# Performance work log

Measured on AMD Instinct MI355X. Metric: run time of the kernel, lower is better.

## Reference

```python
import jax, jax.numpy as jnp
import numpy as np

B, T, D, H, O = 64, 512, 512, 512, 1

def setup_inputs() -> dict:
    key = jax.random.key(0)
    ks = jax.random.split(key, 12)
    s_in = 1.0 / np.sqrt(H)
    inp = {
        'x': jax.random.normal(ks[0], (B, T, D), dtype=jnp.float32),
        'W_ih0': jax.random.uniform(ks[1], (H, D), jnp.float32, -s_in, s_in),
        'W_hh0': jax.random.uniform(ks[2], (H, H), jnp.float32, -s_in, s_in),
        'b_ih0': jax.random.uniform(ks[3], (H,), jnp.float32, -s_in, s_in),
        'b_hh0': jax.random.uniform(ks[4], (H,), jnp.float32, -s_in, s_in),
        'W_ih1': jax.random.uniform(ks[5], (H, H), jnp.float32, -s_in, s_in),
        'W_hh1': jax.random.uniform(ks[6], (H, H), jnp.float32, -s_in, s_in),
        'b_ih1': jax.random.uniform(ks[7], (H,), jnp.float32, -s_in, s_in),
        'b_hh1': jax.random.uniform(ks[8], (H,), jnp.float32, -s_in, s_in),
        'W_fc': jax.random.uniform(ks[9], (O, H), jnp.float32, -s_in, s_in),
        'b_fc': jax.random.uniform(ks[10], (O,), jnp.float32, -s_in, s_in),
    }
    return inp

def _rnn_layer(inp, W_ih, W_hh, b_ih, b_hh):
    # inp: [B, T, Din] -> [B, T, H].  h_t = tanh(x_t W_ih^T + b_ih + h_{t-1} W_hh^T + b_hh)
    xproj = jnp.einsum('btd,hd->bth', inp, W_ih) + b_ih + b_hh  # precompute input projection
    h0 = jnp.zeros((inp.shape[0], W_hh.shape[0]), inp.dtype)
    def step(h, xp):  # xp: [B, H]
        h = jnp.tanh(xp + h @ W_hh.T)
        return h, h
    _, outs = jax.lax.scan(step, h0, jnp.swapaxes(xproj, 0, 1))  # [T, B, H]
    return jnp.swapaxes(outs, 0, 1)

def reference(x, W_ih0, W_hh0, b_ih0, b_hh0, W_ih1, W_hh1, b_ih1, b_hh1, W_fc, b_fc):
    h = _rnn_layer(x, W_ih0, W_hh0, b_ih0, b_hh0)
    h = _rnn_layer(h, W_ih1, W_hh1, b_ih1, b_hh1)
    last = h[:, -1, :]                      # [B, H]
    return last @ W_fc.T + b_fc             # [B, O]
```

## Files before the change

kernel.cpp:

```cpp
#include <hip/hip_runtime.h>
#include <cstdint>
#include <cstddef>

typedef _Float16 f16;
typedef _Float16 half2_t __attribute__((ext_vector_type(2)));
typedef _Float16 half4_t __attribute__((ext_vector_type(4)));
typedef _Float16 half8_t __attribute__((ext_vector_type(8)));
typedef float floatx4 __attribute__((ext_vector_type(4)));

__device__ __forceinline__ float fdot2u(uint32_t w, uint32_t h, float acc) {
#if __has_builtin(__builtin_amdgcn_fdot2)
    return __builtin_amdgcn_fdot2(__builtin_bit_cast(half2_t, w),
                                  __builtin_bit_cast(half2_t, h), acc, false);
#else
    half2_t a = __builtin_bit_cast(half2_t, w);
    half2_t b = __builtin_bit_cast(half2_t, h);
    return acc + (float)a[0] * (float)b[0] + (float)a[1] * (float)b[1];
#endif
}

__device__ __forceinline__ void spin_ge(int* f, int v) {
    while (__hip_atomic_load(f, __ATOMIC_RELAXED, __HIP_MEMORY_SCOPE_AGENT) < v)
        __builtin_amdgcn_s_sleep(16);
}

__global__ void cvt_kernel(const float* __restrict__ in, f16* __restrict__ out, int n4) {
    int i = blockIdx.x * blockDim.x + threadIdx.x;
    int stride = gridDim.x * blockDim.x;
    const float4* in4 = (const float4*)in;
    half4_t* out4 = (half4_t*)out;
    for (; i < n4; i += stride) {
        float4 v = in4[i];
        half4_t h = {(f16)v.x, (f16)v.y, (f16)v.z, (f16)v.w};
        out4[i] = h;
    }
}

__global__ void bsum_kernel(const float* __restrict__ a, const float* __restrict__ b,
                            float* __restrict__ o) {
    int i = threadIdx.x;
    o[i] = a[i] + b[i];
}

__global__ void pack_whh(const float* __restrict__ W, uint32_t* __restrict__ wp) {
    int id = blockIdx.x * 256 + threadIdx.x;
    int j = id >> 8;
    int kp = id & 255;
    int k = kp * 2;
    int w = j >> 6, jsub = (j >> 3) & 7, r = j & 7;
    int kg = k >> 6, c = (k >> 3) & 7, q = (k >> 1) & 3;
    int tid = w * 64 + jsub * 8 + kg;
    int idx = c * 32 + r * 4 + q;
    uint32_t lo = (uint32_t)__builtin_bit_cast(uint16_t, (f16)W[(size_t)j * 512 + k]);
    uint32_t hi = (uint32_t)__builtin_bit_cast(uint16_t, (f16)W[(size_t)j * 512 + k + 1]);
    size_t off;
    if (idx < 224) off = (size_t)idx * 512 + tid;
    else           off = (size_t)224 * 512 + ((size_t)(r * 512 + tid)) * 4 + q;
    wp[off] = (hi << 16) | lo;
}

__global__ __launch_bounds__(256) void gemm_xp(const f16* __restrict__ A,
                                               const f16* __restrict__ Bw,
                                               const float* __restrict__ bias,
                                               f16* __restrict__ C) {
    const int bn = blockIdx.x & 3;
    const int bm = blockIdx.x >> 2;
    const int tid = threadIdx.x;
    const int w = tid >> 6, l = tid & 63;
    const int wr = w >> 1, wc = w & 1;
    __shared__ f16 As[128 * 32];
    __shared__ f16 Bs[128 * 32];
    floatx4 acc[4][4] = {};
    const int lr = l & 15, lk = (l >> 4) * 8;
    for (int kk = 0; kk < 512; kk += 32) {
        __syncthreads();
        uint4 av[2], bv[2];
#pragma unroll
        for (int s = 0; s < 2; ++s) {
            int chunk = tid + s * 256;
            int row = chunk >> 2;
            int colh = (chunk & 3) * 8;
            av[s] = *(const uint4*)&A[((size_t)(bm * 128 + row)) * 512 + kk + colh];
            bv[s] = *(const uint4*)&Bw[((size_t)(bn * 128 + row)) * 512 + kk + colh];
        }
#pragma unroll
        for (int s = 0; s < 2; ++s) {
            int chunk = tid + s * 256;
            *(uint4*)&As[chunk * 8] = av[s];
            *(uint4*)&Bs[chunk * 8] = bv[s];
        }
        __syncthreads();
        half8_t af[4], bf[4];
#pragma unroll
        for (int m = 0; m < 4; ++m)
            af[m] = *(const half8_t*)&As[(wr * 64 + m * 16 + lr) * 32 + lk];
#pragma unroll
        for (int n = 0; n < 4; ++n)
            bf[n] = *(const half8_t*)&Bs[(wc * 64 + n * 16 + lr) * 32 + lk];
#pragma unroll
        for (int m = 0; m < 4; ++m)
#pragma unroll
            for (int n = 0; n < 4; ++n)
                acc[m][n] = __builtin_amdgcn_mfma_f32_16x16x32_f16(af[m], bf[n], acc[m][n], 0, 0, 0);
    }
    float bz[4];
#pragma unroll
    for (int n = 0; n < 4; ++n) bz[n] = bias[bn * 128 + wc * 64 + n * 16 + lr];
    const int lq = l >> 4;
#pragma unroll
    for (int m = 0; m < 4; ++m)
#pragma unroll
        for (int n = 0; n < 4; ++n)
#pragma unroll
            for (int e = 0; e < 4; ++e) {
                int row = bm * 128 + wr * 64 + m * 16 + lq * 4 + e;
                int col = bn * 128 + wc * 64 + n * 16 + lr;
                C[(size_t)row * 512 + col] = (f16)(acc[m][n][e] + bz[n]);
            }
}

#define FOR_Q(M, c, r) M(c, r, 0) M(c, r, 1) M(c, r, 2) M(c, r, 3)
#define FOR_R8(M, c) FOR_Q(M, c, 0) FOR_Q(M, c, 1) FOR_Q(M, c, 2) FOR_Q(M, c, 3) \
                     FOR_Q(M, c, 4) FOR_Q(M, c, 5) FOR_Q(M, c, 6) FOR_Q(M, c, 7)
#define FOR_ALL(M) FOR_R8(M, 0) FOR_R8(M, 1) FOR_R8(M, 2) FOR_R8(M, 3) \
                   FOR_R8(M, 4) FOR_R8(M, 5) FOR_R8(M, 6)

#define DECLW(c, r, q) uint32_t W_##c##_##r##_##q;
#define LOADW(c, r, q) W_##c##_##r##_##q = wpb[(size_t)(((c)*32 + (r)*4 + (q)) * 512) + tid];
#define DOTQ(c, r, q) a##r = fdot2u(W_##c##_##r##_##q, hq##q, a##r);

#define CHUNK(c)                                                   \
    {                                                              \
        uint4 hv = *(const uint4*)(hrow + (c) * 4);                \
        uint32_t hq0 = hv.x, hq1 = hv.y, hq2 = hv.z, hq3 = hv.w;   \
        FOR_R8(DOTQ, c)                                            \
    }

#define LROW(r)                                                    \
    {                                                              \
        uint4 wv = *(const uint4*)&wlds[((r) * 512 + tid) * 4];    \
        a##r = fdot2u(wv.x, hq0, a##r);                            \
        a##r = fdot2u(wv.y, hq1, a##r);                            \
        a##r = fdot2u(wv.z, hq2, a##r);                            \
        a##r = fdot2u(wv.w, hq3, a##r);                            \
    }

#define CHUNKL                                                     \
    {                                                              \
        uint4 hv = *(const uint4*)(hrow + 7 * 4);                  \
        uint32_t hq0 = hv.x, hq1 = hv.y, hq2 = hv.z, hq3 = hv.w;   \
        LROW(0) LROW(1) LROW(2) LROW(3)                            \
        LROW(4) LROW(5) LROW(6) LROW(7)                            \
    }

#define HB_STRIDE 72

__global__ __launch_bounds__(512)
__attribute__((amdgpu_waves_per_eu(2, 2)))
void fused3(const f16* __restrict__ xp0, const uint32_t* __restrict__ wp0,
            const uint32_t* __restrict__ wpih1, const uint32_t* __restrict__ wp1,
            const float* __restrict__ bs1,
            f16* __restrict__ h0seq, f16* __restrict__ xp1seq,
            f16* __restrict__ h1last,
            int* __restrict__ flag1, int* __restrict__ flag2) {
    const int stage = blockIdx.x >> 6;
    const int row = blockIdx.x & 63;
    const int tid = threadIdx.x;
    const int kg = tid & 7;
    __shared__ alignas(16) f16 hbuf[2][8 * HB_STRIDE];
    __shared__ uint32_t wlds[8 * 512 * 4];
    __shared__ alignas(16) f16 xin[2][16 * 512];

    const uint32_t* wpb = (stage == 0) ? wp0 : (stage == 1) ? wpih1 : wp1;
    const f16* inbase = (stage == 0) ? xp0 + (size_t)row * 262144
                       : (stage == 1) ? h0seq + (size_t)row * 262144
                                      : xp1seq + (size_t)row * 262144;
    f16* outbase = (stage == 0) ? h0seq + (size_t)row * 262144
                  : (stage == 1) ? xp1seq + (size_t)row * 262144
                                 : h1last + (size_t)row * 512;
    int* flIn  = (stage == 1) ? flag1 + row : (stage == 2) ? flag2 + row : nullptr;
    int* flOut = (stage == 0) ? flag1 + row : (stage == 1) ? flag2 + row : nullptr;

    auto stageDMA = [&](int g) {
        const char* src = (const char*)inbase + (size_t)g * 16384 + (size_t)tid * 16;
        char* dst = (char*)&xin[g & 1][0] + (tid >> 6) * 1024;
        __builtin_amdgcn_global_load_lds((const uint32_t*)src, (uint32_t*)dst, 16, 0, 0);
        __builtin_amdgcn_global_load_lds((const uint32_t*)(src + 8192),
                                         (uint32_t*)(dst + 8192), 16, 0, 0);
    };

    FOR_ALL(DECLW)
    FOR_ALL(LOADW)
#pragma unroll
    for (int i = 0; i < 8; ++i) {
        uint4 v = *(const uint4*)&wpb[(size_t)224 * 512 + (size_t)(i * 512 + tid) * 4];
        *(uint4*)&wlds[(i * 512 + tid) * 4] = v;
    }
    for (int i = tid; i < 2 * 8 * HB_STRIDE; i += 512) ((f16*)hbuf)[i] = (f16)0.f;
    float bsv = (stage == 1) ? bs1[tid] : 0.f;

    if (flIn) { spin_ge(flIn, 2); __threadfence(); }
    stageDMA(0);
    asm volatile("s_waitcnt vmcnt(0)" ::: "memory");
    __syncthreads();

    const bool m0 = (tid & 1), m1 = (tid & 2), m2 = (tid & 4);
    const int hwpos = (tid >> 6) * HB_STRIDE + (tid & 63);

    for (int t = 0; t < 512; ++t) {
        const int c = t >> 4;
        if ((t & 15) == 4 && c < 31) {
            if (flIn) { spin_ge(flIn, c + 2); __threadfence(); }
            stageDMA(c + 1);
        }

        float xpv;
        if (stage == 1) {
            f16 v = xin[c & 1][(t & 15) * 512 + tid];
            hbuf[t & 1][hwpos] = v;
            __syncthreads();
            if ((t & 15) == 0 && t > 0 && tid == 0) {
                __threadfence();
                __hip_atomic_store(flOut, c, __ATOMIC_RELAXED, __HIP_MEMORY_SCOPE_AGENT);
            }
            xpv = bsv;
        } else {
            xpv = (float)xin[c & 1][(t & 15) * 512 + tid];
        }

        float a0 = 0.f, a1 = 0.f, a2 = 0.f, a3 = 0.f;
        float a4 = 0.f, a5 = 0.f, a6 = 0.f, a7 = 0.f;
        const uint32_t* hrow = (const uint32_t*)&hbuf[t & 1][kg * HB_STRIDE];
        CHUNKL
        CHUNK(0) CHUNK(1) CHUNK(2) CHUNK(3) CHUNK(4) CHUNK(5) CHUNK(6)

        float b0 = (m0 ? a1 : a0) + __shfl_xor(m0 ? a0 : a1, 1);
        float b1 = (m0 ? a3 : a2) + __shfl_xor(m0 ? a2 : a3, 1);
        float b2 = (m0 ? a5 : a4) + __shfl_xor(m0 ? a4 : a5, 1);
        float b3 = (m0 ? a7 : a6) + __shfl_xor(m0 ? a6 : a7, 1);
        float c0 = (m1 ? b1 : b0) + __shfl_xor(m1 ? b0 : b1, 2);
        float c1 = (m1 ? b3 : b2) + __shfl_xor(m1 ? b2 : b3, 2);
        float d0 = (m2 ? c1 : c0) + __shfl_xor(m2 ? c0 : c1, 4);
        float s = d0 + xpv;

        if (stage == 1) {
            outbase[(size_t)t * 512 + tid] = (f16)s;
        } else {
            float e = __expf(2.0f * s);
            f16 hh = (f16)(1.0f - 2.0f / (1.0f + e));
            hbuf[(t + 1) & 1][hwpos] = hh;
            if (stage == 0) outbase[(size_t)t * 512 + tid] = hh;
            else if (t == 511) outbase[tid] = hh;
            __syncthreads();
            if (stage == 0 && (t & 15) == 15 && tid == 0) {
                __threadfence();
                __hip_atomic_store(flOut, c + 1, __ATOMIC_RELAXED, __HIP_MEMORY_SCOPE_AGENT);
            }
        }
    }
    if (stage == 1) {
        __syncthreads();
        if (tid == 0) {
            __threadfence();
            __hip_atomic_store(flOut, 32, __ATOMIC_RELAXED, __HIP_MEMORY_SCOPE_AGENT);
        }
    }
}

__global__ __launch_bounds__(512) void fc_kernel(const f16* __restrict__ h1,
                                                 const float* __restrict__ Wfc,
                                                 const float* __restrict__ bfc,
                                                 float* __restrict__ out) {
    int b = blockIdx.x, tid = threadIdx.x;
    __shared__ float red[8];
    float v = (float)h1[(size_t)b * 512 + tid] * Wfc[tid];
#pragma unroll
    for (int off = 32; off > 0; off >>= 1) v += __shfl_down(v, off, 64);
    if ((tid & 63) == 0) red[tid >> 6] = v;
    __syncthreads();
    if (tid == 0) {
        float s = bfc[0];
#pragma unroll
        for (int g = 0; g < 8; ++g) s += red[g];
        out[b] = s;
    }
}

extern "C" void kernel_launch(void* const* d_in, const int* in_sizes, int n_in,
                              void* d_out, int out_size, void* d_ws, size_t ws_size,
                              hipStream_t stream) {
    const float* x    = (const float*)d_in[0];
    const float* Wih0 = (const float*)d_in[1];
    const float* Whh0 = (const float*)d_in[2];
    const float* bih0 = (const float*)d_in[3];
    const float* bhh0 = (const float*)d_in[4];
    const float* Wih1 = (const float*)d_in[5];
    const float* Whh1 = (const float*)d_in[6];
    const float* bih1 = (const float*)d_in[7];
    const float* bhh1 = (const float*)d_in[8];
    const float* Wfc  = (const float*)d_in[9];
    const float* bfc  = (const float*)d_in[10];
    float* out = (float*)d_out;

    char* ws = (char*)d_ws;
    size_t off = 0;
    auto alloc = [&](size_t bytes) -> void* {
        void* p = ws + off;
        off += (bytes + 255) & ~(size_t)255;
        return p;
    };
    const size_t MTD = (size_t)64 * 512 * 512;
    f16* x16    = (f16*)alloc(MTD * 2);
    f16* h016   = (f16*)alloc(MTD * 2);
    f16* xpb    = (f16*)alloc(MTD * 2);
    f16* xp1b   = (f16*)alloc(MTD * 2);
    f16* wih016 = (f16*)alloc((size_t)512 * 512 * 2);
    uint32_t* wp0   = (uint32_t*)alloc((size_t)131072 * 4);
    uint32_t* wp1   = (uint32_t*)alloc((size_t)131072 * 4);
    uint32_t* wpih1 = (uint32_t*)alloc((size_t)131072 * 4);
    float* bs0 = (float*)alloc(512 * 4);
    float* bs1 = (float*)alloc(512 * 4);
    f16* h1last = (f16*)alloc((size_t)64 * 512 * 2);
    int* flags = (int*)alloc(128 * 4);

    cvt_kernel<<<2048, 256, 0, stream>>>(x, x16, (int)(MTD / 4));
    cvt_kernel<<<256, 256, 0, stream>>>(Wih0, wih016, 512 * 512 / 4);
    bsum_kernel<<<1, 512, 0, stream>>>(bih0, bhh0, bs0);
    bsum_kernel<<<1, 512, 0, stream>>>(bih1, bhh1, bs1);
    pack_whh<<<512, 256, 0, stream>>>(Whh0, wp0);
    pack_whh<<<512, 256, 0, stream>>>(Whh1, wp1);
    pack_whh<<<512, 256, 0, stream>>>(Wih1, wpih1);
    hipMemsetAsync(flags, 0, 128 * 4, stream);

    gemm_xp<<<1024, 256, 0, stream>>>(x16, wih016, bs0, xpb);
    fused3<<<192, 512, 0, stream>>>(xpb, wp0, wpih1, wp1, bs1,
                                    h016, xp1b, h1last, flags, flags + 64);
    fc_kernel<<<64, 512, 0, stream>>>(h1last, Wfc, bfc, out);
}
```

Baseline: 1.323 ms.

## Decouple stage-1 projection from per-step barriers and pad staged input rows

The stage-1 input-projection blocks no longer copy each timestep into hbuf and sync every step. They read the staged chunk directly from LDS and compute all 16 timesteps back to back, signalling downstream once per chunk. Chunk staging moves from async global_load_lds DMA to plain vector loads into a padded row layout (XROW 576), matching the hbuf stride to avoid LDS bank conflicts. The flag protocol shifts: the first wait is on chunk 1, the prefetch point moves to step 12, and staging is now synchronous register loads that may stall the recurrent loop.

```diff
diff --git a/kernel.cpp b/kernel.cpp
--- a/kernel.cpp
+++ b/kernel.cpp
@@ -28,11 +28,10 @@
     int i = blockIdx.x * blockDim.x + threadIdx.x;
     int stride = gridDim.x * blockDim.x;
     const float4* in4 = (const float4*)in;
-    half4_t* out4 = (half4_t*)out;
     for (; i < n4; i += stride) {
         float4 v = in4[i];
         half4_t h = {(f16)v.x, (f16)v.y, (f16)v.z, (f16)v.w};
-        out4[i] = h;
+        *(half4_t*)&out[(size_t)i * 4] = h;
     }
 }
 
@@ -153,7 +152,17 @@
         LROW(4) LROW(5) LROW(6) LROW(7)                            \
     }
 
+#define TREE8                                                                 \
+    float b0 = (m0 ? a1 : a0) + __shfl_xor(m0 ? a0 : a1, 1);                  \
+    float b1 = (m0 ? a3 : a2) + __shfl_xor(m0 ? a2 : a3, 1);                  \
+    float b2 = (m0 ? a5 : a4) + __shfl_xor(m0 ? a4 : a5, 1);                  \
+    float b3 = (m0 ? a7 : a6) + __shfl_xor(m0 ? a6 : a7, 1);                  \
+    float c0 = (m1 ? b1 : b0) + __shfl_xor(m1 ? b0 : b1, 2);                  \
+    float c1 = (m1 ? b3 : b2) + __shfl_xor(m1 ? b2 : b3, 2);                  \
+    float d0 = (m2 ? c1 : c0) + __shfl_xor(m2 ? c0 : c1, 4);
+
 #define HB_STRIDE 72
+#define XROW 576
 
 __global__ __launch_bounds__(512)
 __attribute__((amdgpu_waves_per_eu(2, 2)))
@@ -169,7 +178,7 @@
     const int kg = tid & 7;
     __shared__ alignas(16) f16 hbuf[2][8 * HB_STRIDE];
     __shared__ uint32_t wlds[8 * 512 * 4];
-    __shared__ alignas(16) f16 xin[2][16 * 512];
+    __shared__ alignas(16) f16 xin[2][16 * XROW];
 
     const uint32_t* wpb = (stage == 0) ? wp0 : (stage == 1) ? wpih1 : wp1;
     const f16* inbase = (stage == 0) ? xp0 + (size_t)row * 262144
@@ -181,12 +190,14 @@
     int* flIn  = (stage == 1) ? flag1 + row : (stage == 2) ? flag2 + row : nullptr;
     int* flOut = (stage == 0) ? flag1 + row : (stage == 1) ? flag2 + row : nullptr;
 
-    auto stageDMA = [&](int g) {
-        const char* src = (const char*)inbase + (size_t)g * 16384 + (size_t)tid * 16;
-        char* dst = (char*)&xin[g & 1][0] + (tid >> 6) * 1024;
-        __builtin_amdgcn_global_load_lds((const uint32_t*)src, (uint32_t*)dst, 16, 0, 0);
-        __builtin_amdgcn_global_load_lds((const uint32_t*)(src + 8192),
-                                         (uint32_t*)(dst + 8192), 16, 0, 0);
+    auto stageChunk = [&](int g) {
+#pragma unroll
+        for (int s2 = 0; s2 < 2; ++s2) {
+            int s = tid + s2 * 512;
+            int rw = s >> 6, pos = s & 63;
+            uint4 v = *(const uint4*)&inbase[(size_t)(g * 16 + rw) * 512 + pos * 8];
+            *(uint4*)&xin[g & 1][rw * XROW + (pos >> 3) * 72 + (pos & 7) * 8] = v;
+        }
     };
 
     FOR_ALL(DECLW)
@@ -199,70 +210,62 @@
     for (int i = tid; i < 2 * 8 * HB_STRIDE; i += 512) ((f16*)hbuf)[i] = (f16)0.f;
     float bsv = (stage == 1) ? bs1[tid] : 0.f;
 
-    if (flIn) { spin_ge(flIn, 2); __threadfence(); }
-    stageDMA(0);
-    asm volatile("s_waitcnt vmcnt(0)" ::: "memory");
+    if (flIn) { spin_ge(flIn, 1); __threadfence(); }
+    stageChunk(0);
     __syncthreads();
 
     const bool m0 = (tid & 1), m1 = (tid & 2), m2 = (tid & 4);
     const int hwpos = (tid >> 6) * HB_STRIDE + (tid & 63);
 
-    for (int t = 0; t < 512; ++t) {
-        const int c = t >> 4;
-        if ((t & 15) == 4 && c < 31) {
-            if (flIn) { spin_ge(flIn, c + 2); __threadfence(); }
-            stageDMA(c + 1);
-        }
-
-        float xpv;
-        if (stage == 1) {
-            f16 v = xin[c & 1][(t & 15) * 512 + tid];
-            hbuf[t & 1][hwpos] = v;
+    if (stage == 1) {
+        for (int c = 0; c < 32; ++c) {
+            for (int lt = 0; lt < 16; ++lt) {
+                if (lt == 12 && c < 31) {
+                    spin_ge(flIn, c + 2); __threadfence();
+                    stageChunk(c + 1);
+                }
+                float a0 = 0.f, a1 = 0.f, a2 = 0.f, a3 = 0.f;
+                float a4 = 0.f, a5 = 0.f, a6 = 0.f, a7 = 0.f;
+                const uint32_t* hrow = (const uint32_t*)&xin[c & 1][lt * XROW + kg * 72];
+                CHUNKL
+                CHUNK(0) CHUNK(1) CHUNK(2) CHUNK(3) CHUNK(4) CHUNK(5) CHUNK(6)
+                TREE8
+                outbase[(size_t)(c * 16 + lt) * 512 + tid] = (f16)(d0 + bsv);
+            }
             __syncthreads();
-            if ((t & 15) == 0 && t > 0 && tid == 0) {
+            if (tid == 0) {
                 __threadfence();
-                __hip_atomic_store(flOut, c, __ATOMIC_RELAXED, __HIP_MEMORY_SCOPE_AGENT);
-            }
-            xpv = bsv;
-        } else {
-            xpv = (float)xin[c & 1][(t & 15) * 512 + tid];
-        }
-
-        float a0 = 0.f, a1 = 0.f, a2 = 0.f, a3 = 0.f;
-        float a4 = 0.f, a5 = 0.f, a6 = 0.f, a7 = 0.f;
-        const uint32_t* hrow = (const uint32_t*)&hbuf[t & 1][kg * HB_STRIDE];
-        CHUNKL
-        CHUNK(0) CHUNK(1) CHUNK(2) CHUNK(3) CHUNK(4) CHUNK(5) CHUNK(6)
-
-        float b0 = (m0 ? a1 : a0) + __shfl_xor(m0 ? a0 : a1, 1);
-        float b1 = (m0 ? a3 : a2) + __shfl_xor(m0 ? a2 : a3, 1);
-        float b2 = (m0 ? a5 : a4) + __shfl_xor(m0 ? a4 : a5, 1);
-        float b3 = (m0 ? a7 : a6) + __shfl_xor(m0 ? a6 : a7, 1);
-        float c0 = (m1 ? b1 : b0) + __shfl_xor(m1 ? b0 : b1, 2);
-        float c1 = (m1 ? b3 : b2) + __shfl_xor(m1 ? b2 : b3, 2);
-        float d0 = (m2 ? c1 : c0) + __shfl_xor(m2 ? c0 : c1, 4);
-        float s = d0 + xpv;
-
-        if (stage == 1) {
-            outbase[(size_t)t * 512 + tid] = (f16)s;
-        } else {
+                __hip_atomic_store(flOut, c + 1, __ATOMIC_RELAXED, __HIP_MEMORY_SCOPE_AGENT);
+            }
+        }
+    } else {
+        int p = 0;
+        for (int t = 0; t < 512; ++t) {
+            const int c = t >> 4, lt = t & 15;
+            if (lt == 12 && c < 31) {
+                if (flIn) { spin_ge(flIn, c + 2); __threadfence(); }
+                stageChunk(c + 1);
+            }
+            float xpv = (float)xin[c & 1][lt * XROW + (tid >> 6) * 72 + (tid & 63)];
+
+            float a0 = 0.f, a1 = 0.f, a2 = 0.f, a3 = 0.f;
+            float a4 = 0.f, a5 = 0.f, a6 = 0.f, a7 = 0.f;
+            const uint32_t* hrow = (const uint32_t*)&hbuf[p][kg * HB_STRIDE];
+            CHUNKL
+            CHUNK(0) CHUNK(1) CHUNK(2) CHUNK(3) CHUNK(4) CHUNK(5) CHUNK(6)
+            TREE8
+            float s = d0 + xpv;
             float e = __expf(2.0f * s);
             f16 hh = (f16)(1.0f - 2.0f / (1.0f + e));
-            hbuf[(t + 1) & 1][hwpos] = hh;
+            hbuf[p ^ 1][hwpos] = hh;
             if (stage == 0) outbase[(size_t)t * 512 + tid] = hh;
             else if (t == 511) outbase[tid] = hh;
             __syncthreads();
-            if (stage == 0 && (t & 15) == 15 && tid == 0) {
+            if (stage == 0 && lt == 15 && tid == 0) {
                 __threadfence();
                 __hip_atomic_store(flOut, c + 1, __ATOMIC_RELAXED, __HIP_MEMORY_SCOPE_AGENT);
             }
-        }
-    }
-    if (stage == 1) {
-        __syncthreads();
-        if (tid == 0) {
-            __threadfence();
-            __hip_atomic_store(flOut, 32, __ATOMIC_RELAXED, __HIP_MEMORY_SCOPE_AGENT);
+            p ^= 1;
         }
     }
 }
```

Result: slower. 1.355 ms (+2.4%).
